# Optimization experiments

Hardware: AMD Instinct MI355X
Metric: run time of the kernel (lower is better)

## Reference

```python
import jax, jax.numpy as jnp
import numpy as np

B, S, D = 16, 2000, 512          # batch, seq_len, input_dim
G, K = 2, 320                    # num_groups, num_vars
CV = 256                         # codevector_dim
d = CV // G                      # per-group codevector dim
TAU = 2.0                        # gumbel-softmax temperature (module default)
EPS = 1e-7


def setup_inputs() -> dict:
    key = jax.random.key(0)
    k0, k1, k2, k3, k4 = jax.random.split(key, 5)
    hidden_states = jax.random.normal(k0, (B, S, D), jnp.float32)
    mask_time_indices = jax.random.randint(k1, (B, S), 0, 2) > 0
    W = jax.random.normal(k2, (G * K, D), jnp.float32) * 0.02  # weight_proj
    b = jnp.zeros((G * K,), jnp.float32)
    codevectors = jax.random.uniform(k3, (1, G * K, d), jnp.float32)  # uniform_ init
    u = jax.random.uniform(k4, (B * S * G, K), jnp.float32, minval=1e-6, maxval=1.0 - 1e-6)
    gumbel = -jnp.log(-jnp.log(u))  # standard Gumbel(0,1) noise
    return dict(hidden_states=hidden_states, mask_time_indices=mask_time_indices,
                W=W, b=b, codevectors=codevectors, gumbel=gumbel)


def _compute_perplexity(probs, mask):
    # probs: (B*S, G, K); mask: (B, S) bool
    mask_f = mask.reshape(-1).astype(probs.dtype)[:, None, None]
    marginal = (probs * mask_f).sum(0) / mask_f.sum()          # (G, K)
    return jnp.exp(-jnp.sum(marginal * jnp.log(marginal + EPS), axis=-1)).sum()


def reference(hidden_states, mask_time_indices, W, b, codevectors, gumbel):
    # weight projection: (B, S, G*K)
    logits = jnp.einsum('bsd,vd->bsv', hidden_states, W) + b
    logits = logits.reshape(B * S * G, K)

    # hard gumbel-softmax (training path), straight-through estimator
    y_soft = jax.nn.softmax((logits + gumbel) / TAU, axis=-1)
    idx = jnp.argmax(y_soft, axis=-1)
    y_hard = jax.nn.one_hot(idx, K, dtype=y_soft.dtype)
    codevector_probs = y_hard + y_soft - jax.lax.stop_gradient(y_soft)

    # perplexity from the soft (non-gumbel, non-tempered) distribution
    soft_dist = jax.nn.softmax(logits.reshape(B * S, G, K), axis=-1)
    perplexity = _compute_perplexity(soft_dist, mask_time_indices)

    # weighted sum of codevectors per group; einsum avoids the (B*S, G*K, d) blowup
    cv = codevectors.reshape(G, K, d)
    out = jnp.einsum('ngk,gkd->ngd', codevector_probs.reshape(B * S, G, K), cv)
    out = out.reshape(B, S, G * d)  # (B, S, codevector_dim)
    return out, perplexity
```

## Files before the change

### kernel.cpp

```cpp
#include <hip/hip_runtime.h>

#define NB    16
#define NS    2000
#define ND    512
#define NG    2
#define NK    320
#define NV    640
#define NDCV  128
#define NTOK  32000
#define TAUF  2.0f
#define EPSF  1e-7f

#define TPB      16
#define NTHREADS 640
#define TIE_THR  4.0e-3f

using half8   = __attribute__((ext_vector_type(8))) _Float16;
using half4   = __attribute__((ext_vector_type(4))) _Float16;
using float4v = __attribute__((ext_vector_type(4))) float;

__device__ inline half8 cvt8hi(float4 p0, float4 p1) {
    half8 a;
    a[0] = (_Float16)p0.x; a[1] = (_Float16)p0.y;
    a[2] = (_Float16)p0.z; a[3] = (_Float16)p0.w;
    a[4] = (_Float16)p1.x; a[5] = (_Float16)p1.y;
    a[6] = (_Float16)p1.z; a[7] = (_Float16)p1.w;
    return a;
}

__device__ inline half4 cvt4hi(float4 p) {
    half4 a;
    a[0] = (_Float16)p.x; a[1] = (_Float16)p.y;
    a[2] = (_Float16)p.z; a[3] = (_Float16)p.w;
    return a;
}

__device__ inline bool beats(float za, int ka, float zb, int kb) {
    return (za > zb) || (za == zb && ka < kb);
}

template <int CTRL>
__device__ __forceinline__ float dpp_rorf(float x) {
    return __int_as_float(__builtin_amdgcn_update_dpp(
        __float_as_int(x), __float_as_int(x), CTRL, 0xF, 0xF, false));
}
template <int CTRL>
__device__ __forceinline__ int dpp_rori(int x) {
    return __builtin_amdgcn_update_dpp(x, x, CTRL, 0xF, 0xF, false);
}

__device__ __forceinline__ float qsum16(float s) {
    s += dpp_rorf<0x128>(s);
    s += dpp_rorf<0x124>(s);
    s += dpp_rorf<0x122>(s);
    s += dpp_rorf<0x121>(s);
    return s;
}

__device__ __forceinline__ void qargmax16(float& z1, int& k1) {
    {
        float oz = dpp_rorf<0x128>(z1); int ok = dpp_rori<0x128>(k1);
        if (beats(oz, ok, z1, k1)) { z1 = oz; k1 = ok; }
    }
    {
        float oz = dpp_rorf<0x124>(z1); int ok = dpp_rori<0x124>(k1);
        if (beats(oz, ok, z1, k1)) { z1 = oz; k1 = ok; }
    }
    {
        float oz = dpp_rorf<0x122>(z1); int ok = dpp_rori<0x122>(k1);
        if (beats(oz, ok, z1, k1)) { z1 = oz; k1 = ok; }
    }
    {
        float oz = dpp_rorf<0x121>(z1); int ok = dpp_rori<0x121>(k1);
        if (beats(oz, ok, z1, k1)) { z1 = oz; k1 = ok; }
    }
}

__global__ void k_wsplit(const float* __restrict__ W, half8* __restrict__ W1p) {
    int t = blockIdx.x * 256 + threadIdx.x;
    if (t >= NV * (ND / 8)) return;
    int v  = t % NV;
    int kc = t / NV;
    const float* src = W + (size_t)v * ND + kc * 8;
    float4 p0 = *(const float4*)src;
    float4 p1 = *(const float4*)(src + 4);
    W1p[t] = cvt8hi(p0, p1);
}

#define AROWB 128
__global__ __launch_bounds__(1024, 4) void k_gemm(
    const float* __restrict__ hidden,
    const half8* __restrict__ W1p,
    const float* __restrict__ bvec,
    _Float16* __restrict__ logits)
{
    __shared__ __align__(16) char Abuf[2][64 * AROWB];

    const int t    = threadIdx.x;
    const int lane = t & 63;
    const int w    = t >> 6;
    const int wn   = w & 7;
    const int wm   = w >> 3;
    const int l15  = lane & 15;
    const int l4   = lane >> 4;
    const int n0b  = blockIdx.x * 64;

    const int sm  = t >> 4;
    const int sk4 = t & 15;
    const float* hrow = hidden + (size_t)(n0b + sm) * ND + sk4 * 4;
    const int wbyte = sm * AROWB + ((((sk4 >> 1) ^ (sm & 7)) << 4) | ((sk4 & 1) << 3));

    float4v acc[2][5];
    #pragma unroll
    for (int mt = 0; mt < 2; ++mt)
        #pragma unroll
        for (int nt = 0; nt < 5; ++nt) acc[mt][nt] = (float4v)0.0f;

    {
        float4 p = *(const float4*)(hrow);
        *(half4*)(&Abuf[0][wbyte]) = cvt4hi(p);
    }

    const half8* bbase = W1p + (size_t)l4 * NV + wn * 80 + l15;

    half8 bc[2][5], bn[2][5];
    #pragma unroll
    for (int ks = 0; ks < 2; ++ks)
        #pragma unroll
        for (int nt = 0; nt < 5; ++nt)
            bc[ks][nt] = bbase[(size_t)(ks * 4) * NV + nt * 16];

    __syncthreads();

    for (int c = 0; c < 8; ++c) {
        float4 p;
        if (c < 7) {
            p = *(const float4*)(hrow + (c + 1) * 64);
            #pragma unroll
            for (int ks = 0; ks < 2; ++ks)
                #pragma unroll
                for (int nt = 0; nt < 5; ++nt)
                    bn[ks][nt] = bbase[(size_t)((c + 1) * 8 + ks * 4) * NV + nt * 16];
        }

        const char* base = Abuf[c & 1];
        #pragma unroll
        for (int ks = 0; ks < 2; ++ks) {
            const int xr = ((ks * 4 + l4) ^ (l15 & 7)) << 4;
            half8 fa[2];
            #pragma unroll
            for (int mt = 0; mt < 2; ++mt)
                fa[mt] = *(const half8*)(base + (wm * 32 + mt * 16 + l15) * AROWB + xr);

            #pragma unroll
            for (int nt = 0; nt < 5; ++nt)
                #pragma unroll
                for (int mt = 0; mt < 2; ++mt)
                    acc[mt][nt] = __builtin_amdgcn_mfma_f32_16x16x32_f16(fa[mt], bc[ks][nt], acc[mt][nt], 0, 0, 0);
        }

        if (c < 7) {
            *(half4*)(&Abuf[(c + 1) & 1][wbyte]) = cvt4hi(p);
            #pragma unroll
            for (int ks = 0; ks < 2; ++ks)
                #pragma unroll
                for (int nt = 0; nt < 5; ++nt)
                    bc[ks][nt] = bn[ks][nt];
        }
        __syncthreads();
    }

    #pragma unroll
    for (int nt = 0; nt < 5; ++nt) {
        const int col = wn * 80 + nt * 16 + l15;
        const float bb = bvec[col];
        #pragma unroll
        for (int mt = 0; mt < 2; ++mt) {
            #pragma unroll
            for (int r = 0; r < 4; ++r) {
                const int row = n0b + wm * 32 + mt * 16 + l4 * 4 + r;
                logits[(size_t)row * NV + col] = (_Float16)(acc[mt][nt][r] + bb);
            }
        }
    }
}

#define EPI_BLOCKS  1024
#define EPI_THREADS 256
#define EPI_SLOTS   (EPI_BLOCKS * (EPI_THREADS / 16))
#define NPAIRS      (NTOK * NG)

__global__ __launch_bounds__(EPI_THREADS) void k_epi(
    const _Float16* __restrict__ logits,
    const float* __restrict__ gumbel,
    const int*   __restrict__ mask,
    const float* __restrict__ hidden,
    const float* __restrict__ W,
    const float* __restrict__ bvec,
    const float* __restrict__ codevec,
    float* __restrict__ out,
    float* __restrict__ marg_ws)
{
    __shared__ float marg[NV];
    const int t     = threadIdx.x;
    const int lane  = t & 63;
    const int q     = lane >> 4;
    const int ql    = lane & 15;
    const int wslot = blockIdx.x * (EPI_THREADS / 16) + (t >> 4);
    const int g     = wslot & 1;

    for (int i = t; i < NV; i += EPI_THREADS) marg[i] = 0.f;
    __syncthreads();

    float mreg[5][4] = {};

    int pair = wslot;
    half4  ch[5];
    float4 cg[5];
    int    cm;
    {
        const _Float16* lrow = logits + (size_t)(pair >> 1) * NV + g * NK;
        const float*    grow = gumbel + (size_t)pair * NK;
        #pragma unroll
        for (int j = 0; j < 5; ++j) {
            ch[j] = *(const half4*)(lrow + 64 * j + 4 * ql);
            cg[j] = *(const float4*)(grow + 64 * j + 4 * ql);
        }
        cm = mask[pair >> 1];
    }

    while (true) {
        const int npair = pair + EPI_SLOTS;
        const bool nvalid = npair < NPAIRS;
        half4  nh[5];
        float4 ng[5];
        int    nm = 0;
        if (nvalid) {
            const _Float16* lrow = logits + (size_t)(npair >> 1) * NV + g * NK;
            const float*    grow = gumbel + (size_t)npair * NK;
            #pragma unroll
            for (int j = 0; j < 5; ++j) {
                nh[j] = *(const half4*)(lrow + 64 * j + 4 * ql);
                ng[j] = *(const float4*)(grow + 64 * j + 4 * ql);
            }
            nm = mask[npair >> 1];
        }

        const int n = pair >> 1;

        float lv[5][4];
        #pragma unroll
        for (int j = 0; j < 5; ++j)
            #pragma unroll
            for (int c = 0; c < 4; ++c)
                lv[j][c] = (float)ch[j][c];

        float e[5][4];
        float s = 0.f;
        #pragma unroll
        for (int j = 0; j < 5; ++j) {
            e[j][0] = __expf(lv[j][0]); e[j][1] = __expf(lv[j][1]);
            e[j][2] = __expf(lv[j][2]); e[j][3] = __expf(lv[j][3]);
            s += (e[j][0] + e[j][1]) + (e[j][2] + e[j][3]);
        }
        s = qsum16(s);
        const float pm = (cm != 0) ? (1.0f / s) : 0.0f;
        #pragma unroll
        for (int j = 0; j < 5; ++j)
            #pragma unroll
            for (int c = 0; c < 4; ++c)
                mreg[j][c] = fmaf(e[j][c], pm, mreg[j][c]);

        float z[5][4];
        #pragma unroll
        for (int j = 0; j < 5; ++j) {
            z[j][0] = lv[j][0] + cg[j].x;
            z[j][1] = lv[j][1] + cg[j].y;
            z[j][2] = lv[j][2] + cg[j].z;
            z[j][3] = lv[j][3] + cg[j].w;
        }
        float z1 = -3.4e38f; int k1 = 0;
        #pragma unroll
        for (int j = 0; j < 5; ++j)
            #pragma unroll
            for (int c = 0; c < 4; ++c) {
                const int idx = 64 * j + 4 * ql + c;
                if (z[j][c] > z1) { z1 = z[j][c]; k1 = idx; }
            }
        qargmax16(z1, k1);

        bool flag = false;
        #pragma unroll
        for (int j = 0; j < 5; ++j)
            #pragma unroll
            for (int c = 0; c < 4; ++c) {
                const int idx = 64 * j + 4 * ql + c;
                flag |= (idx != k1) && (z[j][c] >= z1 - TIE_THR);
            }
        const unsigned long long bal = __ballot(flag);
        const unsigned int m16 = (unsigned int)((bal >> (q * 16)) & 0xFFFFull);

        int kbest = k1;
        if (m16) {
            float z2 = -3.4e38f; int k2 = 0x7fffffff;
            #pragma unroll
            for (int j = 0; j < 5; ++j)
                #pragma unroll
                for (int c = 0; c < 4; ++c) {
                    const int idx = 64 * j + 4 * ql + c;
                    const float zz = (idx == k1) ? -3.4e38f : z[j][c];
                    if (zz > z2) { z2 = zz; k2 = idx; }
                }
            #pragma unroll
            for (int off = 1; off < 16; off <<= 1) {
                float oz = __shfl_xor(z2, off, 16);
                int   ok = __shfl_xor(k2, off, 16);
                if (beats(oz, ok, z2, k2)) { z2 = oz; k2 = ok; }
            }
            if (z1 - z2 < TIE_THR) {
                const float* hr  = hidden + (size_t)n * ND;
                const float* w1r = W + ((size_t)g * NK + k1) * ND;
                const float* w2r = W + ((size_t)g * NK + k2) * ND;
                const float* grow = gumbel + (size_t)pair * NK;
                double s1 = 0.0, s2 = 0.0;
                #pragma unroll
                for (int j = 0; j < 32; ++j) {
                    const int idx = ql * 32 + j;
                    const double h = (double)hr[idx];
                    s1 += h * (double)w1r[idx];
                    s2 += h * (double)w2r[idx];
                }
                #pragma unroll
                for (int off = 8; off > 0; off >>= 1) {
                    s1 += __shfl_xor(s1, off, 16);
                    s2 += __shfl_xor(s2, off, 16);
                }
                const double zz1 = s1 + (double)bvec[g * NK + k1] + (double)grow[k1];
                const double zz2 = s2 + (double)bvec[g * NK + k2] + (double)grow[k2];
                const bool firstWins = (zz1 > zz2) || (zz1 == zz2 && k1 < k2);
                kbest = firstWins ? k1 : k2;
            }
        }

        const float4* cvrow = (const float4*)(codevec + ((size_t)g * NK + kbest) * NDCV);
        float4* dst = (float4*)(out + (size_t)n * (NG * NDCV) + g * NDCV);
        dst[ql]      = cvrow[ql];
        dst[ql + 16] = cvrow[ql + 16];

        if (!nvalid) break;
        pair = npair;
        cm = nm;
        #pragma unroll
        for (int j = 0; j < 5; ++j) { ch[j] = nh[j]; cg[j] = ng[j]; }
    }

    #pragma unroll
    for (int j = 0; j < 5; ++j)
        #pragma unroll
        for (int c = 0; c < 4; ++c)
            atomicAdd(&marg[g * NK + 64 * j + 4 * ql + c], mreg[j][c]);
    __syncthreads();
    float* dstm = marg_ws + (size_t)blockIdx.x * NV;
    for (int i = t; i < NV; i += EPI_THREADS) dstm[i] = marg[i];
}

__global__ __launch_bounds__(256) void k_reduce(
    const float* __restrict__ marg_ws, float* __restrict__ marginal)
{
    __shared__ float red[8][32];
    const int v  = blockIdx.x * 32 + (threadIdx.x & 31);
    const int ch = threadIdx.x >> 5;

    float s = 0.f;
    for (int i = 0; i < EPI_BLOCKS / 8; ++i)
        s += marg_ws[(size_t)(ch * (EPI_BLOCKS / 8) + i) * NV + v];

    red[ch][threadIdx.x & 31] = s;
    __syncthreads();
    if (ch == 0) {
        float tot = s;
        #pragma unroll
        for (int c = 1; c < 8; ++c) tot += red[c][threadIdx.x & 31];
        marginal[v] = tot;
    }
}

__global__ __launch_bounds__(NTHREADS) void k_finalize(
    const int* __restrict__ mask,
    const float* __restrict__ marginal,
    float* __restrict__ ppl_out)
{
    __shared__ float red[16];
    const int tid  = threadIdx.x;
    const int wave = tid >> 6;
    const int lane = tid & 63;

    float cnt = 0.f;
    for (int i = tid; i < NTOK; i += NTHREADS) cnt += (mask[i] != 0) ? 1.f : 0.f;
    #pragma unroll
    for (int off = 32; off > 0; off >>= 1) cnt += __shfl_xor(cnt, off);
    if (lane == 0) red[wave] = cnt;
    __syncthreads();
    float total = 0.f;
    #pragma unroll
    for (int wv = 0; wv < 10; wv++) total += red[wv];
    __syncthreads();

    float p = marginal[tid] / total;
    float val = p * logf(p + EPSF);
    #pragma unroll
    for (int off = 32; off > 0; off >>= 1) val += __shfl_xor(val, off);
    if (lane == 0) red[wave] = val;
    __syncthreads();
    if (tid == 0) {
        float h0 = red[0] + red[1] + red[2] + red[3] + red[4];
        float h1 = red[5] + red[6] + red[7] + red[8] + red[9];
        ppl_out[0] = expf(-h0) + expf(-h1);
    }
}

__global__ void k_transpose(const float* __restrict__ W, float* __restrict__ WT) {
    int idx = blockIdx.x * 256 + threadIdx.x;
    if (idx >= ND * NV) return;
    int k = idx / NV;
    int v = idx - k * NV;
    WT[idx] = W[v * ND + k];
}

__global__ __launch_bounds__(NTHREADS) void k_main_fb(
    const float* __restrict__ hidden,
    const int*   __restrict__ mask,
    const float* __restrict__ bvec,
    const float* __restrict__ WT,
    const float* __restrict__ codevec,
    const float* __restrict__ gumbel,
    float* __restrict__ out,
    float* __restrict__ marginal)
{
    __shared__ float smem[TPB * NV];
    __shared__ float marg_lds[NV];

    const int tid = threadIdx.x;
    const int n0  = blockIdx.x * TPB;

    marg_lds[tid] = 0.0f;
    {
        const float4* src = (const float4*)(hidden + (size_t)n0 * ND);
        float4* dst = (float4*)smem;
        for (int i = tid; i < TPB * ND / 4; i += NTHREADS) dst[i] = src[i];
    }
    __syncthreads();

    const int vgroup = tid % 160;
    const int tgroup = tid / 160;
    const int v0 = vgroup * 4;
    const int t0 = tgroup * 4;

    float acc[4][4] = {};
    const float* hbase = smem + t0 * ND;

    for (int k = 0; k < ND; k += 4) {
        float wv_[4][4], h[4][4];
        #pragma unroll
        for (int i = 0; i < 4; i++) {
            float4 tw = *(const float4*)(WT + (size_t)(k + i) * NV + v0);
            wv_[i][0] = tw.x; wv_[i][1] = tw.y; wv_[i][2] = tw.z; wv_[i][3] = tw.w;
        }
        #pragma unroll
        for (int i = 0; i < 4; i++) {
            float4 th = *(const float4*)(hbase + i * ND + k);
            h[i][0] = th.x; h[i][1] = th.y; h[i][2] = th.z; h[i][3] = th.w;
        }
        #pragma unroll
        for (int kk = 0; kk < 4; kk++)
            #pragma unroll
            for (int ti = 0; ti < 4; ti++)
                #pragma unroll
                for (int vi = 0; vi < 4; vi++)
                    acc[ti][vi] = fmaf(h[ti][kk], wv_[kk][vi], acc[ti][vi]);
    }

    __syncthreads();

    #pragma unroll
    for (int ti = 0; ti < 4; ti++) {
        float4 lv;
        lv.x = acc[ti][0] + bvec[v0 + 0];
        lv.y = acc[ti][1] + bvec[v0 + 1];
        lv.z = acc[ti][2] + bvec[v0 + 2];
        lv.w = acc[ti][3] + bvec[v0 + 3];
        *(float4*)(smem + (size_t)(t0 + ti) * NV + v0) = lv;
    }
    __syncthreads();

    const int wave = tid >> 6;
    const int lane = tid & 63;
    const int g = wave & 1;
    float marg_reg[5] = {0.f, 0.f, 0.f, 0.f, 0.f};

    for (int pair = wave; pair < 2 * TPB; pair += 10) {
        const int tt = pair >> 1;
        const int n = n0 + tt;
        const float* lrow = smem + tt * NV + g * NK;

        float lv[5];
        #pragma unroll
        for (int j = 0; j < 5; j++) lv[j] = lrow[lane + 64 * j];

        float m = lv[0];
        #pragma unroll
        for (int j = 1; j < 5; j++) m = fmaxf(m, lv[j]);
        #pragma unroll
        for (int off = 32; off > 0; off >>= 1) m = fmaxf(m, __shfl_xor(m, off));

        float e[5], s = 0.f;
        #pragma unroll
        for (int j = 0; j < 5; j++) { e[j] = expf(lv[j] - m); s += e[j]; }
        #pragma unroll
        for (int off = 32; off > 0; off >>= 1) s += __shfl_xor(s, off);
        const float inv = 1.0f / s;

        if (mask[n] != 0) {
            #pragma unroll
            for (int j = 0; j < 5; j++) marg_reg[j] += e[j] * inv;
        }

        const float* grow = gumbel + ((size_t)n * NG + g) * NK;
        float zbest = -3.4e38f;
        int kbest = 0;
        #pragma unroll
        for (int j = 0; j < 5; j++) {
            float z = lv[j] + grow[lane + 64 * j];
            if (z > zbest) { zbest = z; kbest = lane + 64 * j; }
        }
        #pragma unroll
        for (int off = 32; off > 0; off >>= 1) {
            float zo = __shfl_xor(zbest, off);
            int ko = __shfl_xor(kbest, off);
            if (zo > zbest || (zo == zbest && ko < kbest)) { zbest = zo; kbest = ko; }
        }

        const float2* cvrow = (const float2*)(codevec + ((size_t)g * NK + kbest) * NDCV);
        float2* dstrow = (float2*)(out + (size_t)n * (NG * NDCV) + g * NDCV);
        dstrow[lane] = cvrow[lane];
    }

    #pragma unroll
    for (int j = 0; j < 5; j++)
        atomicAdd(&marg_lds[g * NK + lane + 64 * j], marg_reg[j]);
    __syncthreads();
    atomicAdd(&marginal[tid], marg_lds[tid]);
}

extern "C" void kernel_launch(void* const* d_in, const int* in_sizes, int n_in,
                              void* d_out, int out_size, void* d_ws, size_t ws_size,
                              hipStream_t stream) {
    const float* hidden  = (const float*)d_in[0];
    const int*   mask    = (const int*)  d_in[1];
    const float* W       = (const float*)d_in[2];
    const float* bvec    = (const float*)d_in[3];
    const float* codevec = (const float*)d_in[4];
    const float* gumbel  = (const float*)d_in[5];
    float* out = (float*)d_out;

    float* marginal = (float*)d_ws;

    const size_t off_w1     = 4096;
    const size_t off_logits = 2u * 1024u * 1024u;
    const size_t off_margws = 44u * 1024u * 1024u;
    const size_t need = off_margws + (size_t)EPI_BLOCKS * NV * 4;

    hipMemsetAsync(marginal, 0, NV * sizeof(float), stream);

    if (ws_size >= need) {
        half8*    W1p     = (half8*)((char*)d_ws + off_w1);
        _Float16* logits  = (_Float16*)((char*)d_ws + off_logits);
        float*    marg_ws = (float*)((char*)d_ws + off_margws);

        k_wsplit<<<(NV * (ND / 8) + 255) / 256, 256, 0, stream>>>(W, W1p);
        k_gemm<<<NTOK / 64, 1024, 0, stream>>>(hidden, W1p, bvec, logits);
        k_epi<<<EPI_BLOCKS, EPI_THREADS, 0, stream>>>(logits, gumbel, mask, hidden, W, bvec,
                                                      codevec, out, marg_ws);
        k_reduce<<<NV / 32, 256, 0, stream>>>(marg_ws, marginal);
    } else {
        float* WT = (float*)d_ws + 1024;
        k_transpose<<<(ND * NV + 255) / 256, 256, 0, stream>>>(W, WT);
        k_main_fb<<<NTOK / TPB, NTHREADS, 0, stream>>>(hidden, mask, bvec, WT, codevec,
                                                       gumbel, out, marginal);
    }
    k_finalize<<<1, NTHREADS, 0, stream>>>(mask, marginal, out + (size_t)NTOK * NG * NDCV);
}
```

Measured before the change: 124.1 us.

## Double K-chunk width in GEMM A staging to halve block barriers

```diff
diff --git a/kernel.cpp b/kernel.cpp
--- a/kernel.cpp
+++ b/kernel.cpp
@@ -28,13 +28,6 @@
     return a;
 }
 
-__device__ inline half4 cvt4hi(float4 p) {
-    half4 a;
-    a[0] = (_Float16)p.x; a[1] = (_Float16)p.y;
-    a[2] = (_Float16)p.z; a[3] = (_Float16)p.w;
-    return a;
-}
-
 __device__ inline bool beats(float za, int ka, float zb, int kb) {
     return (za > zb) || (za == zb && ka < kb);
 }
@@ -87,14 +80,14 @@
     W1p[t] = cvt8hi(p0, p1);
 }
 
-#define AROWB 128
+#define AROWB2 256
 __global__ __launch_bounds__(1024, 4) void k_gemm(
     const float* __restrict__ hidden,
     const half8* __restrict__ W1p,
     const float* __restrict__ bvec,
     _Float16* __restrict__ logits)
 {
-    __shared__ __align__(16) char Abuf[2][64 * AROWB];
+    __shared__ __align__(16) char Abuf[2][64 * AROWB2];
 
     const int t    = threadIdx.x;
     const int lane = t & 63;
@@ -106,9 +99,9 @@
     const int n0b  = blockIdx.x * 64;
 
     const int sm  = t >> 4;
-    const int sk4 = t & 15;
-    const float* hrow = hidden + (size_t)(n0b + sm) * ND + sk4 * 4;
-    const int wbyte = sm * AROWB + ((((sk4 >> 1) ^ (sm & 7)) << 4) | ((sk4 & 1) << 3));
+    const int sk8 = t & 15;
+    const float* hrow = hidden + (size_t)(n0b + sm) * ND + sk8 * 8;
+    const int wbyte = sm * AROWB2 + ((sk8 ^ (sm & 15)) << 4);
 
     float4v acc[2][5];
     #pragma unroll
@@ -117,8 +110,9 @@
         for (int nt = 0; nt < 5; ++nt) acc[mt][nt] = (float4v)0.0f;
 
     {
-        float4 p = *(const float4*)(hrow);
-        *(half4*)(&Abuf[0][wbyte]) = cvt4hi(p);
+        float4 p0 = *(const float4*)(hrow);
+        float4 p1 = *(const float4*)(hrow + 4);
+        *(half8*)(&Abuf[0][wbyte]) = cvt8hi(p0, p1);
     }
 
     const half8* bbase = W1p + (size_t)l4 * NV + wn * 80 + l15;
@@ -132,40 +126,68 @@
 
     __syncthreads();
 
-    for (int c = 0; c < 8; ++c) {
-        float4 p;
-        if (c < 7) {
-            p = *(const float4*)(hrow + (c + 1) * 64);
-            #pragma unroll
-            for (int ks = 0; ks < 2; ++ks)
-                #pragma unroll
-                for (int nt = 0; nt < 5; ++nt)
-                    bn[ks][nt] = bbase[(size_t)((c + 1) * 8 + ks * 4) * NV + nt * 16];
-        }
-
-        const char* base = Abuf[c & 1];
+    for (int c2 = 0; c2 < 4; ++c2) {
+        float4 p0, p1;
+        if (c2 < 3) {
+            p0 = *(const float4*)(hrow + (c2 + 1) * 128);
+            p1 = *(const float4*)(hrow + (c2 + 1) * 128 + 4);
+        }
+        const char* base = Abuf[c2 & 1];
+
+        #pragma unroll
+        for (int ks = 0; ks < 2; ++ks)
+            #pragma unroll
+            for (int nt = 0; nt < 5; ++nt)
+                bn[ks][nt] = bbase[(size_t)((2 * c2 + 1) * 8 + ks * 4) * NV + nt * 16];
+
         #pragma unroll
         for (int ks = 0; ks < 2; ++ks) {
-            const int xr = ((ks * 4 + l4) ^ (l15 & 7)) << 4;
+            const int xr = ((ks * 4 + l4) ^ l15) << 4;
             half8 fa[2];
             #pragma unroll
             for (int mt = 0; mt < 2; ++mt)
-                fa[mt] = *(const half8*)(base + (wm * 32 + mt * 16 + l15) * AROWB + xr);
-
+                fa[mt] = *(const half8*)(base + (wm * 32 + mt * 16 + l15) * AROWB2 + xr);
             #pragma unroll
             for (int nt = 0; nt < 5; ++nt)
                 #pragma unroll
                 for (int mt = 0; mt < 2; ++mt)
                     acc[mt][nt] = __builtin_amdgcn_mfma_f32_16x16x32_f16(fa[mt], bc[ks][nt], acc[mt][nt], 0, 0, 0);
         }
-
-        if (c < 7) {
-            *(half4*)(&Abuf[(c + 1) & 1][wbyte]) = cvt4hi(p);
+        #pragma unroll
+        for (int ks = 0; ks < 2; ++ks)
+            #pragma unroll
+            for (int nt = 0; nt < 5; ++nt)
+                bc[ks][nt] = bn[ks][nt];
+
+        if (c2 < 3) {
+            #pragma unroll
+            for (int ks = 0; ks < 2; ++ks)
+                #pragma unroll
+                for (int nt = 0; nt < 5; ++nt)
+                    bn[ks][nt] = bbase[(size_t)((2 * c2 + 2) * 8 + ks * 4) * NV + nt * 16];
+        }
+
+        #pragma unroll
+        for (int ks = 0; ks < 2; ++ks) {
+            const int xr = ((8 + ks * 4 + l4) ^ l15) << 4;
+            half8 fa[2];
+            #pragma unroll
+            for (int mt = 0; mt < 2; ++mt)
+                fa[mt] = *(const half8*)(base + (wm * 32 + mt * 16 + l15) * AROWB2 + xr);
+            #pragma unroll
+            for (int nt = 0; nt < 5; ++nt)
+                #pragma unroll
+                for (int mt = 0; mt < 2; ++mt)
+                    acc[mt][nt] = __builtin_amdgcn_mfma_f32_16x16x32_f16(fa[mt], bc[ks][nt], acc[mt][nt], 0, 0, 0);
+        }
+
+        if (c2 < 3) {
             #pragma unroll
             for (int ks = 0; ks < 2; ++ks)
                 #pragma unroll
                 for (int nt = 0; nt < 5; ++nt)
                     bc[ks][nt] = bn[ks][nt];
+            *(half8*)(&Abuf[(c2 + 1) & 1][wbyte]) = cvt8hi(p0, p1);
         }
         __syncthreads();
     }
```

After: 125.6 us. About the same (+1.2%).
